# Kernel tuning notes

Measured on AMD Instinct MI355X. Metric: run time of the kernel, lower is better.

The kernel has to match this reference:

```python
import jax, jax.numpy as jnp
import numpy as np

B, HS, NS = 4096, 4, 64          # batch, hedge_size, neighbor_samples
T = 32                            # n_types (type_dim == output_dim)
E = 64                            # nodeEmb feature width
N_NODES, N_HEDGES = 100000, 500000


def setup_inputs() -> dict:
    key = jax.random.key(0)
    ks = jax.random.split(key, 8)
    return {
        "neighbors": jax.random.randint(ks[0], (B, HS), 0, N_NODES, dtype=jnp.int64)
            if jax.config.jax_enable_x64 else jax.random.randint(ks[0], (B, HS), 0, N_NODES).astype(jnp.int32),
        "train_hedges": jax.random.randint(ks[1], (B,), 0, N_HEDGES).astype(jnp.int32),
        "labels": jax.random.randint(ks[2], (B,), 0, T).astype(jnp.int32),
        "neighborhedges": jax.random.randint(ks[3], (N_NODES, NS), 0, N_HEDGES).astype(jnp.int32),
        "hedgetypes": jax.random.randint(ks[4], (N_HEDGES,), 0, T).astype(jnp.int32),
        "nodeEmb": jax.random.randint(ks[5], (N_NODES, E), 0, 100).astype(jnp.int32),
        "type_features": jnp.eye(T, dtype=jnp.float32),  # _build_type_feature: identity one-hot table
        "W1": jax.random.normal(ks[6], (T, T), dtype=jnp.float32) * 0.1,
        "b1": jnp.zeros((T,), dtype=jnp.float32),
        "W2": jax.random.normal(ks[7], (E, T), dtype=jnp.float32) * 0.1,
        "b2": jnp.zeros((T,), dtype=jnp.float32),
    }


def reference(neighbors, train_hedges, labels, neighborhedges, hedgetypes, nodeEmb,
              type_features, W1, b1, W2, b2):
    b, hs = neighbors.shape
    ns = neighborhedges.shape[1]
    # _get_neighbors_and_masks: chained gathers
    flat_nodes = neighbors.reshape(-1)
    neighbor_edges = neighborhedges[flat_nodes].reshape(b, hs * ns)      # [B, HS*NS]
    node_emb = nodeEmb[flat_nodes].reshape(b, hs, -1).astype(jnp.float32)  # [B, HS, E]
    mask = (neighbor_edges != train_hedges[:, None]).astype(jnp.float32)  # exclude training hyperedge
    # _aggregate_neighbors: gather types then one-hot type features
    self_vec = type_features[labels]                                      # [B, T]
    types = hedgetypes[neighbor_edges.reshape(-1)]                        # [B*HS*NS]
    nv = type_features[types].reshape(b, hs, ns, -1)                      # [B, HS, NS, T]
    m = mask.reshape(b, hs, ns, 1)
    # MeanAggregator (PathCon-style): masked mean over samples, mean over hedge slots,
    # add self vector, linear layer (identity activation; scores feed CrossEntropyLoss)
    avg = (nv * m).sum(axis=-2) / jnp.maximum(m.sum(axis=-2), 1.0)        # [B, HS, T]
    agg = avg.mean(axis=1) + self_vec                                     # [B, T]
    vector1 = agg @ W1 + b1                                               # [B, T] == scores
    node_feat = node_emb.mean(axis=1) @ W2 + b2                           # [B, T]
    embedding = jnp.concatenate([vector1, node_feat], axis=-1)            # [B, 2T]
    scores = vector1
    scores_normalized = jax.nn.sigmoid(scores)
    return scores, scores_normalized, embedding
```

## Files before the change

### kernel.cpp

```cpp
#include <hip/hip_runtime.h>
#include <hip/hip_bf16.h>

constexpr int HS = 4;
constexpr int NS = 64;
constexpr int T  = 32;
constexpr int E  = 64;

__global__ __launch_bounds__(64)
void polyhype_kernel(const int*   __restrict__ neighbors,
                     const int*   __restrict__ train_hedges,
                     const int*   __restrict__ labels,
                     const int*   __restrict__ neighborhedges,
                     const int*   __restrict__ hedgetypes,
                     const int*   __restrict__ nodeEmb,
                     const float* __restrict__ tf,
                     const float* __restrict__ W1,
                     const float* __restrict__ b1,
                     const float* __restrict__ W2,
                     const float* __restrict__ b2,
                     float*       __restrict__ out,
                     int B)
{
    const int b    = blockIdx.x;
    const int lane = threadIdx.x;

    __shared__ float hist[HS][T];
    __shared__ float embacc[E];
    __shared__ float aggL[T];

    ((float*)hist)[lane]      = 0.f;
    ((float*)hist)[lane + 64] = 0.f;
    __syncthreads();

    const int th = train_hedges[b];

    float den[HS];
    float eacc = 0.f;
    #pragma unroll
    for (int h = 0; h < HS; ++h) {
        const int node = neighbors[b * HS + h];
        const int edge = neighborhedges[node * NS + lane];
        const bool m   = (edge != th);
        const int  ty  = hedgetypes[edge];
        den[h] = fmaxf((float)__popcll(__ballot(m)), 1.0f);
        if (m) atomicAdd(&hist[h][ty], 1.0f);
        eacc += (float)nodeEmb[node * E + lane];
    }
    embacc[lane] = eacc * (1.0f / HS);
    __syncthreads();

    const int t = lane & 31;
    float result;

    if (lane < T) {
        float agg = 0.f;
        #pragma unroll
        for (int h = 0; h < HS; ++h) {
            float s = 0.f;
            #pragma unroll 8
            for (int ty = 0; ty < T; ++ty)
                s += hist[h][ty] * tf[ty * T + t];
            agg += s / den[h];
        }
        agg = agg * (1.0f / HS) + tf[labels[b] * T + t];
        aggL[t] = agg;
    }
    __syncthreads();

    if (lane < T) {
        float v = b1[t];
        #pragma unroll 8
        for (int u = 0; u < T; ++u)
            v += aggL[u] * W1[u * T + t];
        result = v;
    } else {
        float v = b2[t];
        #pragma unroll 8
        for (int e = 0; e < E; ++e)
            v += embacc[e] * W2[e * T + t];
        result = v;
    }

    float* scores = out;
    float* sig    = out + (size_t)B * T;
    float* emb    = out + (size_t)2 * B * T;
    if (lane < T) {
        const float s = result;
        scores[b * T + t] = s;
        sig[b * T + t]    = 1.0f / (1.0f + expf(-s));
        emb[(size_t)b * 2 * T + t] = s;
    } else {
        emb[(size_t)b * 2 * T + T + t] = result;
    }
}

extern "C" void kernel_launch(void* const* d_in, const int* in_sizes, int n_in,
                              void* d_out, int out_size, void* d_ws, size_t ws_size,
                              hipStream_t stream) {
    const int*   neighbors      = (const int*)  d_in[0];
    const int*   train_hedges   = (const int*)  d_in[1];
    const int*   labels         = (const int*)  d_in[2];
    const int*   neighborhedges = (const int*)  d_in[3];
    const int*   hedgetypes     = (const int*)  d_in[4];
    const int*   nodeEmb        = (const int*)  d_in[5];
    const float* tf             = (const float*)d_in[6];
    const float* W1             = (const float*)d_in[7];
    const float* b1             = (const float*)d_in[8];
    const float* W2             = (const float*)d_in[9];
    const float* b2             = (const float*)d_in[10];
    float*       out            = (float*)      d_out;

    const int B = in_sizes[1];

    polyhype_kernel<<<B, 64, 0, stream>>>(
        neighbors, train_hedges, labels, neighborhedges, hedgetypes, nodeEmb,
        tf, W1, b1, W2, b2, out, B);
}
```

Before: 19.62 us.

## Pack four batch rows per block and replace shared atomics with ballot histograms

Each 64-thread wave now handles one batch row, with four waves per 256-thread block. Block-wide syncs become wave barriers. The shared-memory atomic histogram is replaced by per-type ballot/popcount counting. All gathers for the four hedge slots are issued up front to raise memory-level parallelism. This removes the atomic contention, the block syncs and the per-block launch overhead, at the cost of 32×4 ballot iterations per wave and more registers per thread.

New measurement: 20.76 us. 1.06x slower.

```diff
diff --git a/kernel.cpp b/kernel.cpp
--- a/kernel.cpp
+++ b/kernel.cpp
@@ -5,8 +5,9 @@
 constexpr int NS = 64;
 constexpr int T  = 32;
 constexpr int E  = 64;
+constexpr int WAVES = 4;
 
-__global__ __launch_bounds__(64)
+__global__ __launch_bounds__(256)
 void polyhype_kernel(const int*   __restrict__ neighbors,
                      const int*   __restrict__ train_hedges,
                      const int*   __restrict__ labels,
@@ -21,63 +22,72 @@
                      float*       __restrict__ out,
                      int B)
 {
-    const int b    = blockIdx.x;
-    const int lane = threadIdx.x;
+    const int wid  = threadIdx.x >> 6;
+    const int lane = threadIdx.x & 63;
+    const int b    = blockIdx.x * WAVES + wid;
+    if (b >= B) return;
 
-    __shared__ float hist[HS][T];
-    __shared__ float embacc[E];
-    __shared__ float aggL[T];
-
-    ((float*)hist)[lane]      = 0.f;
-    ((float*)hist)[lane + 64] = 0.f;
-    __syncthreads();
+    __shared__ float emb_s[WAVES][E];
+    __shared__ float agg_s[WAVES][T];
 
     const int th = train_hedges[b];
 
-    float den[HS];
+    const int4 nd = ((const int4*)neighbors)[b];
+    int node[HS] = { nd.x, nd.y, nd.z, nd.w };
+
+    int edge[HS];
+    #pragma unroll
+    for (int h = 0; h < HS; ++h)
+        edge[h] = neighborhedges[(size_t)node[h] * NS + lane];
+
+    int ty[HS];
+    #pragma unroll
+    for (int h = 0; h < HS; ++h)
+        ty[h] = hedgetypes[edge[h]];
+
     float eacc = 0.f;
     #pragma unroll
+    for (int h = 0; h < HS; ++h)
+        eacc += (float)nodeEmb[(size_t)node[h] * E + lane];
+    emb_s[wid][lane] = eacc * (1.0f / HS);
+
+    unsigned long long mm[HS];
+    float den[HS];
+    #pragma unroll
     for (int h = 0; h < HS; ++h) {
-        const int node = neighbors[b * HS + h];
-        const int edge = neighborhedges[node * NS + lane];
-        const bool m   = (edge != th);
-        const int  ty  = hedgetypes[edge];
-        den[h] = fmaxf((float)__popcll(__ballot(m)), 1.0f);
-        if (m) atomicAdd(&hist[h][ty], 1.0f);
-        eacc += (float)nodeEmb[node * E + lane];
+        mm[h]  = __ballot(edge[h] != th);
+        den[h] = fmaxf((float)__popcll(mm[h]), 1.0f);
     }
-    embacc[lane] = eacc * (1.0f / HS);
-    __syncthreads();
 
     const int t = lane & 31;
+    float agg = 0.f;
+    #pragma unroll
+    for (int h = 0; h < HS; ++h) {
+        float s = 0.f;
+        #pragma unroll 8
+        for (int k = 0; k < T; ++k) {
+            const float cnt = (float)__popcll(__ballot(ty[h] == k) & mm[h]);
+            s += cnt * tf[k * T + t];
+        }
+        agg += s / den[h];
+    }
+    agg = agg * (1.0f / HS) + tf[labels[b] * T + t];
+    if (lane < T) agg_s[wid][t] = agg;
+
+    __builtin_amdgcn_wave_barrier();
+
     float result;
-
-    if (lane < T) {
-        float agg = 0.f;
-        #pragma unroll
-        for (int h = 0; h < HS; ++h) {
-            float s = 0.f;
-            #pragma unroll 8
-            for (int ty = 0; ty < T; ++ty)
-                s += hist[h][ty] * tf[ty * T + t];
-            agg += s / den[h];
-        }
-        agg = agg * (1.0f / HS) + tf[labels[b] * T + t];
-        aggL[t] = agg;
-    }
-    __syncthreads();
-
     if (lane < T) {
         float v = b1[t];
         #pragma unroll 8
         for (int u = 0; u < T; ++u)
-            v += aggL[u] * W1[u * T + t];
+            v += agg_s[wid][u] * W1[u * T + t];
         result = v;
     } else {
         float v = b2[t];
         #pragma unroll 8
         for (int e = 0; e < E; ++e)
-            v += embacc[e] * W2[e * T + t];
+            v += emb_s[wid][e] * W2[e * T + t];
         result = v;
     }
 
@@ -112,7 +122,8 @@
 
     const int B = in_sizes[1];
 
-    polyhype_kernel<<<B, 64, 0, stream>>>(
+    const int grid = (B + WAVES - 1) / WAVES;
+    polyhype_kernel<<<grid, 256, 0, stream>>>(
         neighbors, train_hedges, labels, neighborhedges, hedgetypes, nodeEmb,
         tf, W1, b1, W2, b2, out, B);
 }
```

## Split hedge slots across four waves and replace shared atomics with ballot counts

Applied to the files above, without the earlier changes.

Each block now runs four wavefronts, one per hedge slot, so the four dependent gather chains (neighborhedges, then hedgetypes, then nodeEmb) are issued in parallel instead of one after another in a single wave. The shared-memory atomic histogram is replaced by 32 ballot+popcount passes that count each type in registers and multiply by the type feature table. The final W1 and W2 linear layers are split between waves 0 and 1, synchronised with wave barriers, and the sigmoid uses the fast __expf. This adds 32 ballot iterations per wave and leaves two waves idle during the epilogue.

Result: faster. 17.04 us (-13.1%).

```diff
diff --git a/kernel.cpp b/kernel.cpp
--- a/kernel.cpp
+++ b/kernel.cpp
@@ -6,7 +6,7 @@
 constexpr int T  = 32;
 constexpr int E  = 64;
 
-__global__ __launch_bounds__(64)
+__global__ __launch_bounds__(256)
 void polyhype_kernel(const int*   __restrict__ neighbors,
                      const int*   __restrict__ train_hedges,
                      const int*   __restrict__ labels,
@@ -22,75 +22,65 @@
                      int B)
 {
     const int b    = blockIdx.x;
-    const int lane = threadIdx.x;
+    const int wid  = threadIdx.x >> 6;
+    const int lane = threadIdx.x & 63;
+    const int t    = lane & 31;
 
-    __shared__ float hist[HS][T];
-    __shared__ float embacc[E];
-    __shared__ float aggL[T];
+    __shared__ float aggp[HS][T];
+    __shared__ float embp[HS][E];
+    __shared__ float emb_mean[E];
+    __shared__ float agg_full[T];
 
-    ((float*)hist)[lane]      = 0.f;
-    ((float*)hist)[lane + 64] = 0.f;
+    const int th   = train_hedges[b];
+    const int node = neighbors[b * HS + wid];
+
+    const int edge = neighborhedges[(size_t)node * NS + lane];
+    const int ty   = hedgetypes[edge];
+    embp[wid][lane] = (float)nodeEmb[(size_t)node * E + lane];
+
+    const unsigned long long mm = __ballot(edge != th);
+    const float rden = 1.0f / fmaxf((float)__popcll(mm), 1.0f);
+
+    float s = 0.f;
+    #pragma unroll
+    for (int k = 0; k < T; ++k) {
+        const float cnt = (float)__popcll(__ballot(ty == k) & mm);
+        s += cnt * tf[k * T + t];
+    }
+    if (lane < T) aggp[wid][t] = s * rden;
+
     __syncthreads();
 
-    const int th = train_hedges[b];
-
-    float den[HS];
-    float eacc = 0.f;
-    #pragma unroll
-    for (int h = 0; h < HS; ++h) {
-        const int node = neighbors[b * HS + h];
-        const int edge = neighborhedges[node * NS + lane];
-        const bool m   = (edge != th);
-        const int  ty  = hedgetypes[edge];
-        den[h] = fmaxf((float)__popcll(__ballot(m)), 1.0f);
-        if (m) atomicAdd(&hist[h][ty], 1.0f);
-        eacc += (float)nodeEmb[node * E + lane];
-    }
-    embacc[lane] = eacc * (1.0f / HS);
-    __syncthreads();
-
-    const int t = lane & 31;
-    float result;
-
-    if (lane < T) {
-        float agg = 0.f;
-        #pragma unroll
-        for (int h = 0; h < HS; ++h) {
-            float s = 0.f;
+    if (wid == 0) {
+        if (lane < T) {
+            float agg = (aggp[0][t] + aggp[1][t] + aggp[2][t] + aggp[3][t]) * 0.25f
+                      + tf[labels[b] * T + t];
+            agg_full[t] = agg;
+        }
+        __builtin_amdgcn_wave_barrier();
+        if (lane < T) {
+            float v = b1[t];
             #pragma unroll 8
-            for (int ty = 0; ty < T; ++ty)
-                s += hist[h][ty] * tf[ty * T + t];
-            agg += s / den[h];
+            for (int u = 0; u < T; ++u)
+                v += agg_full[u] * W1[u * T + t];
+            float* scores = out;
+            float* sig    = out + (size_t)B * T;
+            float* emb    = out + (size_t)2 * B * T;
+            scores[b * T + t] = v;
+            sig[b * T + t]    = 1.0f / (1.0f + __expf(-v));
+            emb[(size_t)b * 2 * T + t] = v;
         }
-        agg = agg * (1.0f / HS) + tf[labels[b] * T + t];
-        aggL[t] = agg;
-    }
-    __syncthreads();
-
-    if (lane < T) {
-        float v = b1[t];
-        #pragma unroll 8
-        for (int u = 0; u < T; ++u)
-            v += aggL[u] * W1[u * T + t];
-        result = v;
-    } else {
-        float v = b2[t];
-        #pragma unroll 8
-        for (int e = 0; e < E; ++e)
-            v += embacc[e] * W2[e * T + t];
-        result = v;
-    }
-
-    float* scores = out;
-    float* sig    = out + (size_t)B * T;
-    float* emb    = out + (size_t)2 * B * T;
-    if (lane < T) {
-        const float s = result;
-        scores[b * T + t] = s;
-        sig[b * T + t]    = 1.0f / (1.0f + expf(-s));
-        emb[(size_t)b * 2 * T + t] = s;
-    } else {
-        emb[(size_t)b * 2 * T + T + t] = result;
+    } else if (wid == 1) {
+        emb_mean[lane] = (embp[0][lane] + embp[1][lane] + embp[2][lane] + embp[3][lane]) * 0.25f;
+        __builtin_amdgcn_wave_barrier();
+        if (lane < T) {
+            float v = b2[t];
+            #pragma unroll 8
+            for (int e = 0; e < E; ++e)
+                v += emb_mean[e] * W2[e * T + t];
+            float* emb = out + (size_t)2 * B * T;
+            emb[(size_t)b * 2 * T + T + t] = v;
+        }
     }
 }
 
@@ -112,7 +102,7 @@
 
     const int B = in_sizes[1];
 
-    polyhype_kernel<<<B, 64, 0, stream>>>(
+    polyhype_kernel<<<B, 256, 0, stream>>>(
         neighbors, train_hedges, labels, neighborhedges, hedgetypes, nodeEmb,
         tf, W1, b1, W2, b2, out, B);
 }
```
